# Kernel tuning notes

Hardware: AMD Instinct MI355X
Metric: run time of the kernel (lower is better)

Reference implementation:

```python
import jax, jax.numpy as jnp
import numpy as np

B, T, D = 2, 2048, 2048
H = 16
HD = D // H  # 128


def _rotate_half(x):
    x1, x2 = x[..., :HD // 2], x[..., HD // 2:]
    return jnp.concatenate((-x2, x1), axis=-1)


def setup_inputs() -> dict:
    key = jax.random.key(0)
    ks = jax.random.split(key, 7)
    return {
        "x": jax.random.normal(ks[0], (B, T, D), dtype=jnp.float32),
        "rope_cos": jax.random.uniform(ks[1], (1, 1, T, HD), dtype=jnp.float32),
        "rope_sin": jax.random.uniform(ks[2], (1, 1, T, HD), dtype=jnp.float32),
        "qkv_w": jax.random.normal(ks[3], (3 * D, D), dtype=jnp.float32) * (1.0 / np.sqrt(D)),
        "qkv_b": jax.random.normal(ks[4], (3 * D,), dtype=jnp.float32) * 0.02,
        "out_w": jax.random.normal(ks[5], (D, D), dtype=jnp.float32) * (1.0 / np.sqrt(D)),
        "out_b": jax.random.normal(ks[6], (D,), dtype=jnp.float32) * 0.02,
    }


def reference(x, rope_cos, rope_sin, qkv_w, qkv_b, out_w, out_b):
    bsz, t, d = x.shape
    # fused QKV projection (torch Linear: x @ W.T + b)
    qkv = x @ qkv_w.T + qkv_b                       # [B, T, 3D]
    qkv = qkv.reshape(bsz, t, 3, H, HD).transpose(2, 0, 3, 1, 4)  # [3, B, H, T, HD]
    q, k, v = qkv[0], qkv[1], qkv[2]
    # RoPE
    cos = rope_cos[:, :, :t, :]
    sin = rope_sin[:, :, :t, :]
    q = q * cos + _rotate_half(q) * sin
    k = k * cos + _rotate_half(k) * sin
    # causal SDPA (eval mode -> no dropout)
    scale = 1.0 / np.sqrt(HD)
    scores = jnp.einsum("bhqd,bhkd->bhqk", q, k) * scale
    causal = jnp.tril(jnp.ones((t, t), dtype=bool))
    scores = jnp.where(causal, scores, jnp.finfo(scores.dtype).min)
    attn = jax.nn.softmax(scores, axis=-1)
    out = jnp.einsum("bhqk,bhkd->bhqd", attn, v)    # [B, H, T, HD]
    out = out.transpose(0, 2, 1, 3).reshape(bsz, t, d)
    return out @ out_w.T + out_b
```

## Files before the change

kernel.cpp:

```cpp
#include <hip/hip_runtime.h>

typedef unsigned short u16;
typedef __attribute__((ext_vector_type(8))) short bf16x8;
typedef __attribute__((ext_vector_type(4))) float f32x4;

__device__ __forceinline__ float bf2f(unsigned int u) {
    union { unsigned int i; float f; } x; x.i = u << 16; return x.f;
}
__device__ __forceinline__ u16 f2bf(float f) {
    union { float f; unsigned int i; } x; x.f = f;
    unsigned int r = x.i + 0x7fffu + ((x.i >> 16) & 1u);
    return (u16)(r >> 16);
}

__device__ __forceinline__ void gl2lds16(const u16* g, u16* l) {
    __builtin_amdgcn_global_load_lds(
        (const __attribute__((address_space(1))) unsigned int*)g,
        (__attribute__((address_space(3))) unsigned int*)l, 16, 0, 0);
}

#define NX  8388608
#define NW1 12582912
#define NW2 4194304
__global__ __launch_bounds__(256) void convert_kernel(
    const float* __restrict__ x, const float* __restrict__ w1,
    const float* __restrict__ w2, u16* __restrict__ dst)
{
    const int i = (blockIdx.x * 256 + threadIdx.x) * 4;
    const float* src;
    int off;
    if (i < NX)            { src = x;  off = i; }
    else if (i < NX + NW1) { src = w1; off = i - NX; }
    else                   { src = w2; off = i - NX - NW1; }
    float4 v = *(const float4*)(src + off);
    ushort4 o;
    o.x = f2bf(v.x); o.y = f2bf(v.y); o.z = f2bf(v.z); o.w = f2bf(v.w);
    *(ushort4*)(dst + i) = o;
}

#define NTILES 64
#define BUFSZ  12288

#define GEMM_SETUP(Ag, Bg)                                                    \
    const int tid = threadIdx.x;                                              \
    const int wave = tid >> 6, lane = tid & 63;                               \
    const int l16 = lane & 15, quad = lane >> 4;                              \
    const int wr = wave >> 2, wc = wave & 3;                                  \
    f32x4 acc[4][4];                                                          \
    _Pragma("unroll") for (int mi = 0; mi < 4; ++mi)                          \
        _Pragma("unroll") for (int ni = 0; ni < 4; ++ni)                      \
            acc[mi][ni] = (f32x4){0.f, 0.f, 0.f, 0.f};                        \
    int aoff[4], boff[4];                                                     \
    _Pragma("unroll") for (int mi = 0; mi < 4; ++mi) {                        \
        const int r = wr * 64 + mi * 16 + l16;                                \
        aoff[mi] = r * 32 + ((quad ^ ((r >> 1) & 3)) << 3);                   \
    }                                                                         \
    _Pragma("unroll") for (int ni = 0; ni < 4; ++ni) {                        \
        const int r = (wc >> 1) * 128 + (ni >> 1) * 64 + (wc & 1) * 32        \
                    + (ni & 1) * 16 + l16;                                    \
        boff[ni] = 4096 + r * 32 + ((quad ^ ((r >> 1) & 3)) << 3);            \
    }                                                                         \
    const u16* sbase[3]; int sdst[3];                                         \
    _Pragma("unroll") for (int j = 0; j < 3; ++j) {                           \
        const int c = wave * 3 + j;                                           \
        const int g = lane & 3;                                               \
        int r; const u16* bp; int d;                                          \
        if (c < 8) {                                                          \
            r = c * 16 + (lane >> 2);                                         \
            bp = Ag + (size_t)(m0 + r) * 2048;                                \
            d = c * 512 + lane * 8;                                           \
        } else {                                                              \
            r = (c - 8) * 16 + (lane >> 2);                                   \
            bp = Bg + (size_t)(n0 + r) * 2048;                                \
            d = 4096 + (c - 8) * 512 + lane * 8;                              \
        }                                                                     \
        sbase[j] = bp + ((g ^ ((r >> 1) & 3)) << 3);                          \
        sdst[j] = d;                                                          \
    }                                                                         \
               \
    _Pragma("unroll") for (int t = 0; t < 3; ++t)                             \
        _Pragma("unroll") for (int j = 0; j < 3; ++j)                         \
            gl2lds16(sbase[j] + t * 32, lds + t * BUFSZ + sdst[j]);           \
    asm volatile("s_waitcnt vmcnt(6)" ::: "memory");                          \
    __builtin_amdgcn_s_barrier();

#define GEMM_PHASE(T, STAGE, VM)                                              \
    {                                                                         \
        u16* buf = lds + ((T) & 3) * BUFSZ;                                   \
        bf16x8 af[4], bf[4];                                                  \
        _Pragma("unroll") for (int mi = 0; mi < 4; ++mi)                      \
            af[mi] = *(const bf16x8*)(buf + aoff[mi]);                        \
        _Pragma("unroll") for (int ni = 0; ni < 4; ++ni)                      \
            bf[ni] = *(const bf16x8*)(buf + boff[ni]);                        \
        if (STAGE) {                                                          \
            u16* nbuf = lds + (((T) + 3) & 3) * BUFSZ;                        \
            _Pragma("unroll") for (int j = 0; j < 3; ++j)                     \
                gl2lds16(sbase[j] + ((T) + 3) * 32, nbuf + sdst[j]);          \
        }                                                                     \
        asm volatile("s_waitcnt vmcnt(" #VM ")" ::: "memory");                \
        __builtin_amdgcn_s_barrier();                                         \
        asm volatile("s_waitcnt lgkmcnt(0)" ::: "memory");                    \
        __builtin_amdgcn_sched_barrier(0);                                    \
        __builtin_amdgcn_s_setprio(1);                                        \
        _Pragma("unroll") for (int mi = 0; mi < 4; ++mi)                      \
            _Pragma("unroll") for (int ni = 0; ni < 4; ++ni)                  \
                acc[mi][ni] = __builtin_amdgcn_mfma_f32_16x16x32_bf16(        \
                    af[mi], bf[ni], acc[mi][ni], 0, 0, 0);                    \
        __builtin_amdgcn_s_setprio(0);                                        \
        __builtin_amdgcn_sched_barrier(0);                                    \
        __builtin_amdgcn_s_barrier();                                         \
    }

#define GEMM_MAIN()                                                           \
    for (int t = 0; t < NTILES - 3; ++t) GEMM_PHASE(t, 1, 6);                 \
    GEMM_PHASE(NTILES - 3, 0, 3);                                             \
    GEMM_PHASE(NTILES - 2, 0, 0);                                             \
    GEMM_PHASE(NTILES - 1, 0, 0);

__global__ __launch_bounds__(512, 2) void qkv8_kernel(
    const u16* __restrict__ xb, const u16* __restrict__ wb,
    const float* __restrict__ bias, const float* __restrict__ rc,
    const float* __restrict__ rs, u16* __restrict__ Qo,
    u16* __restrict__ Ko, u16* __restrict__ Vo)
{
    __shared__ u16 lds[4 * BUFSZ];
    const int bid = blockIdx.x;
    const int swz = (bid & 7) * 96 + (bid >> 3);
    const int m0 = (swz & 31) * 128;
    const int n0 = (swz >> 5) * 256;

    GEMM_SETUP(xb, wb)
    GEMM_MAIN()

    const int e  = n0 >> 11;
    const int h  = ((n0 & 2047) >> 7) + (wc >> 1);
    const int hb = n0 + (wc >> 1) * 128;
    const int hq = wc & 1;
    if (e < 2) {
        u16* dst = (e == 0) ? Qo : Ko;
        #pragma unroll
        for (int mi = 0; mi < 4; ++mi) {
            #pragma unroll
            for (int r = 0; r < 4; ++r) {
                const int m = m0 + wr * 64 + mi * 16 + quad * 4 + r;
                const int b = m >> 11, tt = m & 2047;
                u16* drow = dst + ((size_t)(b * 16 + h) * 2048 + tt) * 128;
                const float* crow = rc + tt * 128;
                const float* sr   = rs + tt * 128;
                #pragma unroll
                for (int p = 0; p < 2; ++p) {
                    const int hd1 = hq * 32 + p * 16 + l16;
                    const int hd2 = hd1 + 64;
                    const float v1 = acc[mi][p][r]     + bias[hb + hd1];
                    const float v2 = acc[mi][p + 2][r] + bias[hb + hd2];
                    drow[hd1] = f2bf(v1 * crow[hd1] - v2 * sr[hd1]);
                    drow[hd2] = f2bf(v2 * crow[hd2] + v1 * sr[hd2]);
                }
            }
        }
    } else {
        #pragma unroll
        for (int mi = 0; mi < 4; ++mi) {
            const int mb = m0 + wr * 64 + mi * 16 + quad * 4;
            const int b = mb >> 11, tt = mb & 2047;
            u16* vbase = Vo + (size_t)(b * 16 + h) * 128 * 2048 + tt;
            #pragma unroll
            for (int ni = 0; ni < 4; ++ni) {
                const int hd = (ni >> 1) * 64 + hq * 32 + (ni & 1) * 16 + l16;
                const float bs = bias[hb + hd];
                ushort4 o;
                #pragma unroll
                for (int r = 0; r < 4; ++r)
                    ((u16*)&o)[r] = f2bf(acc[mi][ni][r] + bs);
                *(ushort4*)(vbase + (size_t)hd * 2048) = o;
            }
        }
    }
}

#define KPAD 136
#define VPAD 72
#define PPAD 72

__global__ __launch_bounds__(256) void attn_mfma_kernel(
    const u16* __restrict__ Qi, const u16* __restrict__ Ki,
    const u16* __restrict__ Vg, u16* __restrict__ Oo)
{
    __shared__ u16 Ks[64 * KPAD];
    __shared__ u16 Vt[128 * VPAD];
    __shared__ u16 Ps[4][16 * PPAD];

    const int tid  = threadIdx.x;
    const int wave = tid >> 6, lane = tid & 63;
    const int l16 = lane & 15, quad = lane >> 4;
    const int bh = blockIdx.y;
    const size_t base = (size_t)bh * (2048 * 128);

    const int qtile[2] = { (int)blockIdx.x, 31 - (int)blockIdx.x };

    bf16x8 qf[2][4];
    f32x4 o[2][8];
    float l_i[2][4];
    #pragma unroll
    for (int s = 0; s < 2; ++s) {
        const u16* qp = Qi + base + (size_t)(qtile[s] * 64 + wave * 16 + l16) * 128 + quad * 8;
        #pragma unroll
        for (int c = 0; c < 4; ++c) qf[s][c] = *(const bf16x8*)(qp + c * 32);
        #pragma unroll
        for (int i = 0; i < 8; ++i) o[s][i] = (f32x4){0.f, 0.f, 0.f, 0.f};
        #pragma unroll
        for (int r = 0; r < 4; ++r) l_i[s][r] = 0.f;
    }

    const float scale = 0.08838834764831845f;
    const int ntiles = qtile[1] + 1;

    for (int t = 0; t < ntiles; ++t) {
        const int kt = t * 64;
        __syncthreads();
        {
            const int key = tid >> 2, d0 = (tid & 3) * 32;
            const u16* src = Ki + base + (size_t)(kt + key) * 128 + d0;
            u16* dst = Ks + key * KPAD + d0;
            #pragma unroll
            for (int i = 0; i < 4; ++i)
                *(bf16x8*)(dst + 8 * i) = *(const bf16x8*)(src + 8 * i);
        }
        {
            const int d = tid >> 1, koff = (tid & 1) * 32;
            const u16* src = Vg + ((size_t)bh * 128 + d) * 2048 + kt + koff;
            u16* dst = Vt + d * VPAD + koff;
            #pragma unroll
            for (int i = 0; i < 4; ++i)
                *(bf16x8*)(dst + 8 * i) = *(const bf16x8*)(src + 8 * i);
        }
        __syncthreads();

        const bool act_a = (t <= qtile[0]);

        f32x4 sa[4], sb[4];
        #pragma unroll
        for (int nt = 0; nt < 4; ++nt) {
            sa[nt] = (f32x4){0.f, 0.f, 0.f, 0.f};
            sb[nt] = (f32x4){0.f, 0.f, 0.f, 0.f};
            #pragma unroll
            for (int c = 0; c < 4; ++c) {
                bf16x8 kf = *(const bf16x8*)(Ks + (nt * 16 + l16) * KPAD + c * 32 + quad * 8);
                sb[nt] = __builtin_amdgcn_mfma_f32_16x16x32_bf16(qf[1][c], kf, sb[nt], 0, 0, 0);
                sa[nt] = __builtin_amdgcn_mfma_f32_16x16x32_bf16(qf[0][c], kf, sa[nt], 0, 0, 0);
            }
        }

        #pragma unroll
        for (int s = 0; s < 2; ++s) {
            if (s == 0 && !act_a) continue;
            f32x4* sc = (s == 0) ? sa : sb;
            const int qrow = qtile[s] * 64 + wave * 16 + quad * 4;
            const bool diag = (t == qtile[s]);

            #pragma unroll
            for (int nt = 0; nt < 4; ++nt) {
                #pragma unroll
                for (int r = 0; r < 4; ++r) {
                    float v = sc[nt][r] * scale - 11.0f;
                    if (diag) {
                        const int key = kt + nt * 16 + l16;
                        v = (key <= qrow + r) ? v : -1.0e30f;
                    }
                    const float e = __expf(v);
                    sc[nt][r] = e;
                    l_i[s][r] += e;
                }
            }

            u16* pw = Ps[wave];
            #pragma unroll
            for (int nt = 0; nt < 4; ++nt)
                #pragma unroll
                for (int r = 0; r < 4; ++r)
                    pw[(quad * 4 + r) * PPAD + nt * 16 + l16] = f2bf(sc[nt][r]);

            bf16x8 pf0 = *(const bf16x8*)(pw + l16 * PPAD + quad * 8);
            bf16x8 pf1 = *(const bf16x8*)(pw + l16 * PPAD + 32 + quad * 8);

            #pragma unroll
            for (int nt = 0; nt < 8; ++nt) {
                bf16x8 vf0 = *(const bf16x8*)(Vt + (nt * 16 + l16) * VPAD + quad * 8);
                bf16x8 vf1 = *(const bf16x8*)(Vt + (nt * 16 + l16) * VPAD + 32 + quad * 8);
                o[s][nt] = __builtin_amdgcn_mfma_f32_16x16x32_bf16(pf0, vf0, o[s][nt], 0, 0, 0);
                o[s][nt] = __builtin_amdgcn_mfma_f32_16x16x32_bf16(pf1, vf1, o[s][nt], 0, 0, 0);
            }
        }
    }

    const int b = bh >> 4, h = bh & 15;
    #pragma unroll
    for (int s = 0; s < 2; ++s) {
        const int qrow = qtile[s] * 64 + wave * 16 + quad * 4;
        #pragma unroll
        for (int r = 0; r < 4; ++r) {
            float ls = l_i[s][r];
            ls += __shfl_xor(ls, 1, 16);
            ls += __shfl_xor(ls, 2, 16);
            ls += __shfl_xor(ls, 4, 16);
            ls += __shfl_xor(ls, 8, 16);
            const float inv = 1.f / ls;
            u16* orow = Oo + ((size_t)(b * 2048 + qrow + r)) * 2048 + h * 128 + l16;
            #pragma unroll
            for (int nt = 0; nt < 8; ++nt)
                orow[nt * 16] = f2bf(o[s][nt][r] * inv);
        }
    }
}

__global__ __launch_bounds__(512, 2) void proj8_kernel(
    const u16* __restrict__ A, const u16* __restrict__ wb,
    const float* __restrict__ bias, float* __restrict__ out)
{
    __shared__ u16 lds[4 * BUFSZ];
    const int bid = blockIdx.x;
    const int swz = (bid & 7) * 32 + (bid >> 3);
    const int m0 = (swz & 31) * 128;
    const int n0 = (swz >> 5) * 256;

    GEMM_SETUP(A, wb)
    GEMM_MAIN()

    #pragma unroll
    for (int mi = 0; mi < 4; ++mi) {
        #pragma unroll
        for (int r = 0; r < 4; ++r) {
            const int m = m0 + wr * 64 + mi * 16 + quad * 4 + r;
            float* orow = out + (size_t)m * 2048;
            #pragma unroll
            for (int ni = 0; ni < 4; ++ni) {
                const int n = n0 + (wc >> 1) * 128 + (ni >> 1) * 64
                            + (wc & 1) * 32 + (ni & 1) * 16 + l16;
                orow[n] = acc[mi][ni][r] + bias[n];
            }
        }
    }
}

extern "C" void kernel_launch(void* const* d_in, const int* in_sizes, int n_in,
                              void* d_out, int out_size, void* d_ws, size_t ws_size,
                              hipStream_t stream) {
    const float* x     = (const float*)d_in[0];
    const float* rcos  = (const float*)d_in[1];
    const float* rsin  = (const float*)d_in[2];
    const float* qkv_w = (const float*)d_in[3];
    const float* qkv_b = (const float*)d_in[4];
    const float* out_w = (const float*)d_in[5];
    const float* out_b = (const float*)d_in[6];
    float* out = (float*)d_out;

    const size_t NE = (size_t)2 * 16 * 2048 * 128;
    u16* Q      = (u16*)d_ws;
    u16* K      = Q + NE;
    u16* V      = K + NE;
    u16* xb     = V + NE;
    u16* O      = xb;
    u16* qkv_wb = xb + NX;
    u16* out_wb = qkv_wb + NW1;

    convert_kernel<<<dim3((NX + NW1 + NW2) / 1024), 256, 0, stream>>>(
        x, qkv_w, out_w, xb);
    qkv8_kernel<<<dim3(768), 512, 0, stream>>>(
        xb, qkv_wb, qkv_b, rcos, rsin, Q, K, V);
    attn_mfma_kernel<<<dim3(16, 32), 256, 0, stream>>>(Q, K, V, O);
    proj8_kernel<<<dim3(256), 512, 0, stream>>>(O, out_wb, out_b, out);
}
```

Before: 378.6 us.

## Deepen GEMM LDS pipeline to six stages and double-buffer register fragments

The shared GEMM main loop for the QKV and output-projection kernels now uses a six-slot LDS ring with five tiles prefetched instead of a four-slot ring with three. Register fragments are double-buffered, so the next tile's LDS reads are issued between the two halves of the current tile's MFMAs, and one barrier per phase is removed. The aim is to hide global-load and LDS-read latency behind matrix math. In exchange, LDS use per block rises by half and more registers are held live, which may cut occupancy under the 512-thread, 2-blocks-per-CU launch bound.

```diff
diff --git a/kernel.cpp b/kernel.cpp
--- a/kernel.cpp
+++ b/kernel.cpp
@@ -77,45 +77,63 @@
         sbase[j] = bp + ((g ^ ((r >> 1) & 3)) << 3);                          \
         sdst[j] = d;                                                          \
     }                                                                         \
-               \
-    _Pragma("unroll") for (int t = 0; t < 3; ++t)                             \
+          \
+    _Pragma("unroll") for (int pt = 0; pt < 5; ++pt)                          \
         _Pragma("unroll") for (int j = 0; j < 3; ++j)                         \
-            gl2lds16(sbase[j] + t * 32, lds + t * BUFSZ + sdst[j]);           \
-    asm volatile("s_waitcnt vmcnt(6)" ::: "memory");                          \
-    __builtin_amdgcn_s_barrier();
-
-#define GEMM_PHASE(T, STAGE, VM)                                              \
+            gl2lds16(sbase[j] + pt * 32, lds + pt * BUFSZ + sdst[j]);         \
+    bf16x8 afr[2][4], bfr[2][4];                                              \
+    asm volatile("s_waitcnt vmcnt(9)" ::: "memory");                          \
+    __builtin_amdgcn_s_barrier();                                             \
+    _Pragma("unroll") for (int mi = 0; mi < 4; ++mi)                          \
+        afr[0][mi] = *(const bf16x8*)(lds + aoff[mi]);                        \
+    _Pragma("unroll") for (int ni = 0; ni < 4; ++ni)                          \
+        bfr[0][ni] = *(const bf16x8*)(lds + boff[ni]);
+
+#define GEMM_PHASE(T, P, STAGE, VM, LOADNEXT)                                 \
     {                                                                         \
-        u16* buf = lds + ((T) & 3) * BUFSZ;                                   \
-        bf16x8 af[4], bf[4];                                                  \
-        _Pragma("unroll") for (int mi = 0; mi < 4; ++mi)                      \
-            af[mi] = *(const bf16x8*)(buf + aoff[mi]);                        \
-        _Pragma("unroll") for (int ni = 0; ni < 4; ++ni)                      \
-            bf[ni] = *(const bf16x8*)(buf + boff[ni]);                        \
         if (STAGE) {                                                          \
-            u16* nbuf = lds + (((T) + 3) & 3) * BUFSZ;                        \
+            u16* nbuf = lds + sw * BUFSZ;                                     \
             _Pragma("unroll") for (int j = 0; j < 3; ++j)                     \
-                gl2lds16(sbase[j] + ((T) + 3) * 32, nbuf + sdst[j]);          \
+                gl2lds16(sbase[j] + ((T) + 5) * 32, nbuf + sdst[j]);          \
         }                                                                     \
         asm volatile("s_waitcnt vmcnt(" #VM ")" ::: "memory");                \
-        __builtin_amdgcn_s_barrier();                                         \
         asm volatile("s_waitcnt lgkmcnt(0)" ::: "memory");                    \
         __builtin_amdgcn_sched_barrier(0);                                    \
         __builtin_amdgcn_s_setprio(1);                                        \
-        _Pragma("unroll") for (int mi = 0; mi < 4; ++mi)                      \
+        _Pragma("unroll") for (int mi = 0; mi < 2; ++mi)                      \
             _Pragma("unroll") for (int ni = 0; ni < 4; ++ni)                  \
                 acc[mi][ni] = __builtin_amdgcn_mfma_f32_16x16x32_bf16(        \
-                    af[mi], bf[ni], acc[mi][ni], 0, 0, 0);                    \
+                    afr[P][mi], bfr[P][ni], acc[mi][ni], 0, 0, 0);            \
+        if (LOADNEXT) {                                                       \
+            const u16* rb = lds + sr * BUFSZ;                                 \
+            _Pragma("unroll") for (int mi = 0; mi < 4; ++mi)                  \
+                afr[(P) ^ 1][mi] = *(const bf16x8*)(rb + aoff[mi]);           \
+            _Pragma("unroll") for (int ni = 0; ni < 4; ++ni)                  \
+                bfr[(P) ^ 1][ni] = *(const bf16x8*)(rb + boff[ni]);           \
+        }                                                                     \
+        _Pragma("unroll") for (int mi = 2; mi < 4; ++mi)                      \
+            _Pragma("unroll") for (int ni = 0; ni < 4; ++ni)                  \
+                acc[mi][ni] = __builtin_amdgcn_mfma_f32_16x16x32_bf16(        \
+                    afr[P][mi], bfr[P][ni], acc[mi][ni], 0, 0, 0);            \
         __builtin_amdgcn_s_setprio(0);                                        \
         __builtin_amdgcn_sched_barrier(0);                                    \
         __builtin_amdgcn_s_barrier();                                         \
+        sr = (sr == 5) ? 0 : sr + 1;                                          \
+        sw = (sw == 5) ? 0 : sw + 1;                                          \
     }
 
 #define GEMM_MAIN()                                                           \
-    for (int t = 0; t < NTILES - 3; ++t) GEMM_PHASE(t, 1, 6);                 \
-    GEMM_PHASE(NTILES - 3, 0, 3);                                             \
-    GEMM_PHASE(NTILES - 2, 0, 0);                                             \
-    GEMM_PHASE(NTILES - 1, 0, 0);
+    int sr = 1, sw = 5;                                                       \
+    for (int t = 0; t < 58; t += 2) {                                         \
+        GEMM_PHASE(t,     0, 1, 9, 1)                                         \
+        GEMM_PHASE(t + 1, 1, 1, 9, 1)                                         \
+    }                                                                         \
+    GEMM_PHASE(58, 0, 1, 9, 1)                                                \
+    GEMM_PHASE(59, 1, 0, 6, 1)                                                \
+    GEMM_PHASE(60, 0, 0, 3, 1)                                                \
+    GEMM_PHASE(61, 1, 0, 0, 1)                                                \
+    GEMM_PHASE(62, 0, 0, 0, 1)                                                \
+    GEMM_PHASE(63, 1, 0, 0, 0)
 
 __global__ __launch_bounds__(512, 2) void qkv8_kernel(
     const u16* __restrict__ xb, const u16* __restrict__ wb,
@@ -123,7 +141,7 @@
     const float* __restrict__ rs, u16* __restrict__ Qo,
     u16* __restrict__ Ko, u16* __restrict__ Vo)
 {
-    __shared__ u16 lds[4 * BUFSZ];
+    __shared__ u16 lds[6 * BUFSZ];
     const int bid = blockIdx.x;
     const int swz = (bid & 7) * 96 + (bid >> 3);
     const int m0 = (swz & 31) * 128;
@@ -146,15 +164,15 @@
                 const int b = m >> 11, tt = m & 2047;
                 u16* drow = dst + ((size_t)(b * 16 + h) * 2048 + tt) * 128;
                 const float* crow = rc + tt * 128;
-                const float* sr   = rs + tt * 128;
+                const float* sr2  = rs + tt * 128;
                 #pragma unroll
                 for (int p = 0; p < 2; ++p) {
                     const int hd1 = hq * 32 + p * 16 + l16;
                     const int hd2 = hd1 + 64;
                     const float v1 = acc[mi][p][r]     + bias[hb + hd1];
                     const float v2 = acc[mi][p + 2][r] + bias[hb + hd2];
-                    drow[hd1] = f2bf(v1 * crow[hd1] - v2 * sr[hd1]);
-                    drow[hd2] = f2bf(v2 * crow[hd2] + v1 * sr[hd2]);
+                    drow[hd1] = f2bf(v1 * crow[hd1] - v2 * sr2[hd1]);
+                    drow[hd2] = f2bf(v2 * crow[hd2] + v1 * sr2[hd2]);
                 }
             }
         }
@@ -317,7 +335,7 @@
     const u16* __restrict__ A, const u16* __restrict__ wb,
     const float* __restrict__ bias, float* __restrict__ out)
 {
-    __shared__ u16 lds[4 * BUFSZ];
+    __shared__ u16 lds[6 * BUFSZ];
     const int bid = blockIdx.x;
     const int swz = (bid & 7) * 32 + (bid >> 3);
     const int m0 = (swz & 31) * 128;
```

Result: no change. 380.8 us (+0.6%).
